# Kernel optimization log

Hardware: AMD Instinct MI355X
Metric: run time of the kernel (lower is better)

## Reference

```python
import jax, jax.numpy as jnp
import numpy as np

B, W = 256, 512
FEAT, TIME, OV_IN, OV = 128, 32, 32, 32
IN = FEAT + TIME + OV  # 192
HG, HL = 256, 128
OG, OL = 128, 64


def _p(key, shape, scale):
    return (jax.random.normal(key, shape, dtype=jnp.float32) * scale)


def setup_inputs() -> dict:
    key = jax.random.key(0)
    ks = jax.random.split(key, 24)
    d = {
        'f_seq': jax.random.normal(ks[0], (B, W, FEAT), dtype=jnp.float32),
        'delta_seq': jax.random.normal(ks[1], (B, W, TIME), dtype=jnp.float32),
        'overlap_seq': jax.random.normal(ks[2], (B, W, OV_IN), dtype=jnp.float32),
        # overlap encoder: Linear(32,64) -> SiLU -> Linear(64,32)
        'W1': _p(ks[3], (64, OV_IN), 1.0 / np.sqrt(OV_IN)),
        'b1': _p(ks[4], (64,), 0.02),
        'W2': _p(ks[5], (OV, 64), 1.0 / np.sqrt(64)),
        'b2': _p(ks[6], (OV,), 0.02),
        # global GRUCell (PyTorch layout: [r; z; n] stacked)
        'Wih_g': _p(ks[7], (3 * HG, IN), 1.0 / np.sqrt(HG)),
        'Whh_g': _p(ks[8], (3 * HG, HG), 1.0 / np.sqrt(HG)),
        'bih_g': _p(ks[9], (3 * HG,), 0.02),
        'bhh_g': _p(ks[10], (3 * HG,), 0.02),
        # local GRUCell
        'Wih_l': _p(ks[11], (3 * HL, IN), 1.0 / np.sqrt(HL)),
        'Whh_l': _p(ks[12], (3 * HL, HL), 1.0 / np.sqrt(HL)),
        'bih_l': _p(ks[13], (3 * HL,), 0.02),
        'bhh_l': _p(ks[14], (3 * HL,), 0.02),
        # output projections
        'Wg': _p(ks[15], (OG, HG), 1.0 / np.sqrt(HG)),
        'bg': _p(ks[16], (OG,), 0.02),
        'Wl': _p(ks[17], (OL, HL), 1.0 / np.sqrt(HL)),
        'bl': _p(ks[18], (OL,), 0.02),
    }
    return d


def _gru_scan(x_ih_seq, h0, Whh, bhh):
    # x_ih_seq: (W, B, 3H) precomputed input gates; returns hidden states (W, B, H)
    def step(h, xih):
        gh = h @ Whh.T + bhh
        xr, xz, xn = jnp.split(xih, 3, axis=-1)
        hr, hz, hn = jnp.split(gh, 3, axis=-1)
        r = jax.nn.sigmoid(xr + hr)
        z = jax.nn.sigmoid(xz + hz)
        n = jnp.tanh(xn + r * hn)
        h_new = (1.0 - z) * n + z * h
        return h_new, h_new
    _, hs = jax.lax.scan(step, h0, x_ih_seq)
    return hs


def _forward(f_seq, delta_seq, overlap_seq, W1, b1, W2, b2,
             Wih_g, Whh_g, bih_g, bhh_g, Wih_l, Whh_l, bih_l, bhh_l,
             Wg, bg, Wl, bl):
    # overlap encoder applied to whole sequence (time-independent)
    ov = jax.nn.silu(overlap_seq @ W1.T + b1) @ W2.T + b2  # (B, W, OV)
    inp = jnp.concatenate([f_seq, delta_seq, ov], axis=-1)  # (B, W, IN)
    # precompute input-to-hidden gates for all timesteps (batched GEMM)
    xih_g = (inp @ Wih_g.T + bih_g).transpose(1, 0, 2)  # (W, B, 3HG)
    xih_l = (inp @ Wih_l.T + bih_l).transpose(1, 0, 2)  # (W, B, 3HL)
    h_g0 = jnp.zeros((inp.shape[0], Whh_g.shape[1]), dtype=inp.dtype)
    h_l0 = jnp.zeros((inp.shape[0], Whh_l.shape[1]), dtype=inp.dtype)
    hg_seq = _gru_scan(xih_g, h_g0, Whh_g, bhh_g)  # (W, B, HG)
    hl_seq = _gru_scan(xih_l, h_l0, Whh_l, bhh_l)  # (W, B, HL)
    g_seq = (hg_seq @ Wg.T + bg).transpose(1, 0, 2)  # (B, W, OG)
    m_seq = (hl_seq @ Wl.T + bl).transpose(1, 0, 2)  # (B, W, OL)
    return g_seq, m_seq


def reference(f_seq, delta_seq, overlap_seq, W1, b1, W2, b2,
              Wih_g, Whh_g, bih_g, bhh_g, Wih_l, Whh_l, bih_l, bhh_l,
              Wg, bg, Wl, bl):
    return _forward(f_seq, delta_seq, overlap_seq, W1, b1, W2, b2,
                    Wih_g, Whh_g, bih_g, bhh_g, Wih_l, Whh_l, bih_l, bhh_l,
                    Wg, bg, Wl, bl)
```

## Files before the change

### kernel.cpp

```cpp
#include <hip/hip_runtime.h>

typedef _Float16 f16;
typedef _Float16 f16x2 __attribute__((ext_vector_type(2)));
typedef _Float16 f16x8 __attribute__((ext_vector_type(8)));
typedef float f32x4 __attribute__((ext_vector_type(4)));
typedef unsigned int u32;

static constexpr size_t NROWS = 131072;
static constexpr int TC = 64;
static constexpr int NCHUNK = 8;
static constexpr size_t CROWS = 256 * TC;

static constexpr size_t O_INP = 0;
static constexpr size_t SZ_INP = NROWS * 192 * 2;
static constexpr size_t O_XB  = O_INP + SZ_INP;
static constexpr size_t SZ_XB = CROWS * 1152 * 2;
static constexpr size_t O_HG  = O_XB + SZ_XB;
static constexpr size_t SZ_HG = NROWS * 256 * 2;
static constexpr size_t O_HL  = O_HG + SZ_HG;
static constexpr size_t SZ_HL = NROWS * 128 * 2;
static constexpr size_t O_WF  = O_HL + SZ_HL;
static constexpr size_t SZ_WF = 1152 * 192 * 2;
static constexpr size_t O_BF  = O_WF + SZ_WF;
static constexpr size_t SZ_BF = 1152 * 4;
static constexpr size_t O_WHG = O_BF + SZ_BF;
static constexpr size_t SZ_WHG = 128 * 768 * 4;
static constexpr size_t O_WHL = O_WHG + SZ_WHG;
static constexpr size_t SZ_WHL = 64 * 384 * 4;
static constexpr size_t O_WG  = O_WHL + SZ_WHL;
static constexpr size_t SZ_WG = 128 * 256 * 2;
static constexpr size_t O_WL  = O_WG + SZ_WG;
static constexpr size_t SZ_WL = 64 * 128 * 2;
static constexpr size_t O_HGF = O_WL + SZ_WL;
static constexpr size_t SZ_HGF = 256 * 256 * 4;
static constexpr size_t O_HGP = O_HGF + SZ_HGF;
static constexpr size_t SZ_HGP = 256 * 128 * 4;
static constexpr size_t O_HLF = O_HGP + SZ_HGP;
static constexpr size_t SZ_HLF = 256 * 128 * 4;
static constexpr size_t O_HLP = O_HLF + SZ_HLF;
static constexpr size_t SZ_HLP = 256 * 64 * 4;
static constexpr size_t WS_NEED = O_HLP + SZ_HLP;

__device__ inline u32 pk2f(float lo, float hi) {
  f16x2 t; t.x = (f16)lo; t.y = (f16)hi;
  return __builtin_bit_cast(u32, t);
}

#if defined(__has_builtin)
#if __has_builtin(__builtin_amdgcn_fdot2)
#define HAVE_FDOT2 1
#endif
#endif

__device__ inline float dot2f(u32 w, u32 h, float c) {
#ifdef HAVE_FDOT2
  return __builtin_amdgcn_fdot2(__builtin_bit_cast(f16x2, w),
                                __builtin_bit_cast(f16x2, h), c, false);
#else
  f16x2 a = __builtin_bit_cast(f16x2, w);
  f16x2 b = __builtin_bit_cast(f16x2, h);
  return c + (float)a.x * (float)b.x + (float)a.y * (float)b.y;
#endif
}

__device__ inline float sigf(float x) { return 1.f / (1.f + __expf(-x)); }
__device__ inline float tanhf_fast(float x) { return 1.f - 2.f / (1.f + __expf(2.f * x)); }

__global__ void prep_k(const float* __restrict__ Wih_g, const float* __restrict__ Wih_l,
                       const float* __restrict__ bih_g, const float* __restrict__ bih_l,
                       const float* __restrict__ Whh_g, const float* __restrict__ Whh_l,
                       const float* __restrict__ Wg, const float* __restrict__ Wl,
                       f16* __restrict__ wfused, float* __restrict__ biasf,
                       u32* __restrict__ whhg, u32* __restrict__ whhl,
                       f16* __restrict__ wg16, f16* __restrict__ wl16) {
  const int tid = blockIdx.x * blockDim.x + threadIdx.x;
  const int stride = gridDim.x * blockDim.x;
  for (int i = tid; i < 1152 * 192; i += stride) {
    int r = i / 192;
    wfused[i] = (f16)(r < 768 ? Wih_g[i] : Wih_l[i - 768 * 192]);
  }
  for (int i = tid; i < 1152; i += stride)
    biasf[i] = (i < 768) ? bih_g[i] : bih_l[i - 768];
  for (int i = tid; i < 128 * 768; i += stride) {
    int k2 = i / 768, r = i % 768;
    whhg[i] = pk2f(Whh_g[r * 256 + 2 * k2], Whh_g[r * 256 + 2 * k2 + 1]);
  }
  for (int i = tid; i < 64 * 384; i += stride) {
    int k2 = i / 384, r = i % 384;
    whhl[i] = pk2f(Whh_l[r * 128 + 2 * k2], Whh_l[r * 128 + 2 * k2 + 1]);
  }
  for (int i = tid; i < 128 * 256; i += stride) wg16[i] = (f16)Wg[i];
  for (int i = tid; i < 64 * 128; i += stride) wl16[i] = (f16)Wl[i];
}

__global__ __launch_bounds__(256) void copy_f_k(const float* __restrict__ f_seq,
                                                f16* __restrict__ inp) {
  const size_t idx = (size_t)blockIdx.x * 256 + threadIdx.x;
  const float4 v = reinterpret_cast<const float4*>(f_seq)[idx];
  const size_t row = idx >> 5, c4 = idx & 31;
  uint2 pr; pr.x = pk2f(v.x, v.y); pr.y = pk2f(v.z, v.w);
  *reinterpret_cast<uint2*>(reinterpret_cast<u32*>(inp) + row * 96 + 2 * c4) = pr;
}

__global__ __launch_bounds__(256) void copy_d_k(const float* __restrict__ delta,
                                                f16* __restrict__ inp) {
  const size_t idx = (size_t)blockIdx.x * 256 + threadIdx.x;
  const float4 v = reinterpret_cast<const float4*>(delta)[idx];
  const size_t row = idx >> 3, c4 = idx & 7;
  uint2 pr; pr.x = pk2f(v.x, v.y); pr.y = pk2f(v.z, v.w);
  *reinterpret_cast<uint2*>(reinterpret_cast<u32*>(inp) + row * 96 + 64 + 2 * c4) = pr;
}

__global__ __launch_bounds__(256) void ovenc_k(
    const float* __restrict__ ovin, const float* __restrict__ W1,
    const float* __restrict__ b1, const float* __restrict__ W2,
    const float* __restrict__ b2, f16* __restrict__ inp) {
  __shared__ float sW1[2048], sW2[2048], sb1[64], sb2[32];
  for (int i = threadIdx.x; i < 2048; i += 256) { sW1[i] = W1[i]; sW2[i] = W2[i]; }
  if (threadIdx.x < 64) sb1[threadIdx.x] = b1[threadIdx.x];
  if (threadIdx.x < 32) sb2[threadIdx.x] = b2[threadIdx.x];
  __syncthreads();
  const size_t row = (size_t)blockIdx.x * 256 + threadIdx.x;

  float ov[32];
  const float4* ovp = reinterpret_cast<const float4*>(ovin + row * 32);
#pragma unroll
  for (int i = 0; i < 8; ++i) {
    float4 v = ovp[i];
    ov[4 * i] = v.x; ov[4 * i + 1] = v.y; ov[4 * i + 2] = v.z; ov[4 * i + 3] = v.w;
  }
  float hb[64];
#pragma unroll
  for (int j = 0; j < 64; ++j) {
    float s = sb1[j];
#pragma unroll
    for (int k = 0; k < 32; ++k) s += sW1[j * 32 + k] * ov[k];
    hb[j] = s * sigf(s);
  }
  u32* orow = reinterpret_cast<u32*>(inp) + row * 96 + 80;
#pragma unroll
  for (int p = 0; p < 16; ++p) {
    float s0 = sb2[2 * p], s1 = sb2[2 * p + 1];
#pragma unroll
    for (int j = 0; j < 64; ++j) {
      s0 += sW2[(2 * p) * 64 + j] * hb[j];
      s1 += sW2[(2 * p + 1) * 64 + j] * hb[j];
    }
    orow[p] = pk2f(s0, s1);
  }
}

template <int K, int NROWSB, int NVALID, bool OUTF16, int LDC, bool REMAP>
__global__ __launch_bounds__(256, 2) void gemm_f16k(
    const f16* __restrict__ A, const f16* __restrict__ Bw,
    const float* __restrict__ bias, void* __restrict__ Cout, int t_base) {
  __shared__ alignas(16) f16 At[128 * 40];
  __shared__ alignas(16) f16 Bt[128 * 40];
  const int n0 = blockIdx.x * 128;
  const int m0 = blockIdx.y * 128;
  const int tid = threadIdx.x;
  const int l = tid & 63;
  const int w = tid >> 6;
  const int wm = w >> 1, wn = w & 1;
  const int srow = tid >> 2, schunk = tid & 3;

  f32x4 acc[4][4] = {};

  for (int k0 = 0; k0 < K; k0 += 32) {
#pragma unroll
    for (int hh = 0; hh < 2; ++hh) {
      int row = srow + hh * 64;
      int m = m0 + row;
      size_t g = REMAP ? ((size_t)(m & 255) * 512 + (size_t)t_base + (size_t)(m >> 8))
                       : (size_t)m;
      uint4 av = *reinterpret_cast<const uint4*>(A + g * K + k0 + schunk * 8);
      *reinterpret_cast<uint4*>(&At[row * 40 + schunk * 8]) = av;
      int nr = n0 + row;
      uint4 bv = make_uint4(0u, 0u, 0u, 0u);
      if (nr < NROWSB)
        bv = *reinterpret_cast<const uint4*>(Bw + (size_t)nr * K + k0 + schunk * 8);
      *reinterpret_cast<uint4*>(&Bt[row * 40 + schunk * 8]) = bv;
    }
    __syncthreads();
    f16x8 af[4], bf[4];
#pragma unroll
    for (int i = 0; i < 4; ++i) {
      af[i] = *reinterpret_cast<const f16x8*>(&At[(wm * 64 + i * 16 + (l & 15)) * 40 + (l >> 4) * 8]);
      bf[i] = *reinterpret_cast<const f16x8*>(&Bt[(wn * 64 + i * 16 + (l & 15)) * 40 + (l >> 4) * 8]);
    }
#pragma unroll
    for (int mi = 0; mi < 4; ++mi)
#pragma unroll
      for (int ni = 0; ni < 4; ++ni)
        acc[mi][ni] = __builtin_amdgcn_mfma_f32_16x16x32_f16(af[mi], bf[ni], acc[mi][ni], 0, 0, 0);
    __syncthreads();
  }

  const int mbase = m0 + wm * 64 + ((l >> 4) << 2);
  const int nbase = n0 + wn * 64 + (l & 15);
#pragma unroll
  for (int mi = 0; mi < 4; ++mi) {
#pragma unroll
    for (int ni = 0; ni < 4; ++ni) {
      int n = nbase + ni * 16;
      if (n < NVALID) {
        float bsv = bias[n];
#pragma unroll
        for (int q = 0; q < 4; ++q) {
          int m = mbase + mi * 16 + q;
          float v = acc[mi][ni][q] + bsv;
          if constexpr (OUTF16)
            reinterpret_cast<f16*>(Cout)[(size_t)m * LDC + n] = (f16)v;
          else
            reinterpret_cast<float*>(Cout)[(size_t)m * LDC + n] = v;
        }
      }
    }
  }
}

__global__ __launch_bounds__(768, 3) void gru_global_k(
    const u32* __restrict__ whh, const float* __restrict__ bhh,
    const f16* __restrict__ xbuf, u32* __restrict__ hseq,
    float* __restrict__ hstf, u32* __restrict__ hstp, int t0) {
  __shared__ alignas(16) u32 hpk[128];
  __shared__ float hfs[256];
  __shared__ float rz[512];
  const int b = blockIdx.x;
  const int r = threadIdx.x;

  u32 wv[128];
#pragma unroll
  for (int i = 0; i < 128; ++i) wv[i] = whh[i * 768 + r];
  const float bh = bhh[r];

  if (t0 == 0) {
    if (r < 256) hfs[r] = 0.f;
    if (r < 128) hpk[r] = 0u;
  } else {
    if (r < 256) hfs[r] = hstf[b * 256 + r];
    if (r < 128) hpk[r] = hstp[b * 128 + r];
  }
  __syncthreads();

  const f16* xp = xbuf + (size_t)b * 1152 + r;
  u32* hout = hseq + (size_t)b * 512 * 128 + (size_t)t0 * 128;
  float xv = (float)xp[0];

  for (int t = 0; t < TC; ++t) {
    float xnext = 0.f;
    if (t < TC - 1) xnext = (float)xp[(size_t)(t + 1) * 256 * 1152];

    float a0 = 0.f, a1 = 0.f, a2 = 0.f, a3 = 0.f;
#pragma unroll
    for (int q = 0; q < 32; ++q) {
      uint4 hq = reinterpret_cast<const uint4*>(hpk)[q];
      a0 = dot2f(wv[4 * q + 0], hq.x, a0);
      a1 = dot2f(wv[4 * q + 1], hq.y, a1);
      a2 = dot2f(wv[4 * q + 2], hq.z, a2);
      a3 = dot2f(wv[4 * q + 3], hq.w, a3);
    }
    float gh = ((a0 + a1) + (a2 + a3)) + bh;

    if (r < 512) rz[r] = sigf(xv + gh);
    __syncthreads();
    if (r >= 512) {
      int j = r - 512;
      float rv = rz[j];
      float zv = rz[256 + j];
      float nv = tanhf_fast(xv + rv * gh);
      float hold = hfs[j];
      float hnew = (1.f - zv) * nv + zv * hold;
      hfs[j] = hnew;
      float hpart = __shfl_xor(hnew, 1, 64);
      if ((j & 1) == 0) {
        u32 packed = pk2f(hnew, hpart);
        hpk[j >> 1] = packed;
        hout[(size_t)t * 128 + (j >> 1)] = packed;
      }
    }
    __syncthreads();
    xv = xnext;
  }
  if (r < 256) hstf[b * 256 + r] = hfs[r];
  if (r < 128) hstp[b * 128 + r] = hpk[r];
}

__global__ __launch_bounds__(384, 2) void gru_local_k(
    const u32* __restrict__ whh, const float* __restrict__ bhh,
    const f16* __restrict__ xbuf, u32* __restrict__ hseq,
    float* __restrict__ hstf, u32* __restrict__ hstp, int t0) {
  __shared__ alignas(16) u32 hpk[64];
  __shared__ float hfs[128];
  __shared__ float rz[256];
  const int b = blockIdx.x;
  const int r = threadIdx.x;

  u32 wv[64];
#pragma unroll
  for (int i = 0; i < 64; ++i) wv[i] = whh[i * 384 + r];
  const float bh = bhh[r];

  if (t0 == 0) {
    if (r < 128) hfs[r] = 0.f;
    if (r < 64) hpk[r] = 0u;
  } else {
    if (r < 128) hfs[r] = hstf[b * 128 + r];
    if (r < 64) hpk[r] = hstp[b * 64 + r];
  }
  __syncthreads();

  const f16* xp = xbuf + (size_t)b * 1152 + 768 + r;
  u32* hout = hseq + (size_t)b * 512 * 64 + (size_t)t0 * 64;
  float xv = (float)xp[0];

  for (int t = 0; t < TC; ++t) {
    float xnext = 0.f;
    if (t < TC - 1) xnext = (float)xp[(size_t)(t + 1) * 256 * 1152];

    float a0 = 0.f, a1 = 0.f, a2 = 0.f, a3 = 0.f;
#pragma unroll
    for (int q = 0; q < 16; ++q) {
      uint4 hq = reinterpret_cast<const uint4*>(hpk)[q];
      a0 = dot2f(wv[4 * q + 0], hq.x, a0);
      a1 = dot2f(wv[4 * q + 1], hq.y, a1);
      a2 = dot2f(wv[4 * q + 2], hq.z, a2);
      a3 = dot2f(wv[4 * q + 3], hq.w, a3);
    }
    float gh = ((a0 + a1) + (a2 + a3)) + bh;

    if (r < 256) rz[r] = sigf(xv + gh);
    __syncthreads();
    if (r >= 256) {
      int j = r - 256;
      float rv = rz[j];
      float zv = rz[128 + j];
      float nv = tanhf_fast(xv + rv * gh);
      float hold = hfs[j];
      float hnew = (1.f - zv) * nv + zv * hold;
      hfs[j] = hnew;
      float hpart = __shfl_xor(hnew, 1, 64);
      if ((j & 1) == 0) {
        u32 packed = pk2f(hnew, hpart);
        hpk[j >> 1] = packed;
        hout[(size_t)t * 64 + (j >> 1)] = packed;
      }
    }
    __syncthreads();
    xv = xnext;
  }
  if (r < 128) hstf[b * 128 + r] = hfs[r];
  if (r < 64) hstp[b * 64 + r] = hpk[r];
}

extern "C" void kernel_launch(void* const* d_in, const int* in_sizes, int n_in,
                              void* d_out, int out_size, void* d_ws, size_t ws_size,
                              hipStream_t stream) {
  (void)in_sizes; (void)n_in; (void)out_size;
  if (ws_size < WS_NEED) return;
  const float* f_seq = (const float*)d_in[0];
  const float* delta = (const float*)d_in[1];
  const float* ovseq = (const float*)d_in[2];
  const float* W1 = (const float*)d_in[3];
  const float* b1 = (const float*)d_in[4];
  const float* W2 = (const float*)d_in[5];
  const float* b2 = (const float*)d_in[6];
  const float* Wih_g = (const float*)d_in[7];
  const float* Whh_g = (const float*)d_in[8];
  const float* bih_g = (const float*)d_in[9];
  const float* bhh_g = (const float*)d_in[10];
  const float* Wih_l = (const float*)d_in[11];
  const float* Whh_l = (const float*)d_in[12];
  const float* bih_l = (const float*)d_in[13];
  const float* bhh_l = (const float*)d_in[14];
  const float* Wg = (const float*)d_in[15];
  const float* bg = (const float*)d_in[16];
  const float* Wl = (const float*)d_in[17];
  const float* bl = (const float*)d_in[18];

  char* ws = (char*)d_ws;
  f16* inp = (f16*)(ws + O_INP);
  f16* xbuf = (f16*)(ws + O_XB);
  f16* hg16 = (f16*)(ws + O_HG);
  f16* hl16 = (f16*)(ws + O_HL);
  f16* wfused = (f16*)(ws + O_WF);
  float* biasf = (float*)(ws + O_BF);
  u32* whhg = (u32*)(ws + O_WHG);
  u32* whhl = (u32*)(ws + O_WHL);
  f16* wg16 = (f16*)(ws + O_WG);
  f16* wl16 = (f16*)(ws + O_WL);
  float* hgf = (float*)(ws + O_HGF);
  u32* hgp = (u32*)(ws + O_HGP);
  float* hlf = (float*)(ws + O_HLF);
  u32* hlp = (u32*)(ws + O_HLP);

  float* outg = (float*)d_out;
  float* outm = outg + NROWS * 128;

  prep_k<<<dim3(256), dim3(256), 0, stream>>>(Wih_g, Wih_l, bih_g, bih_l, Whh_g, Whh_l,
                                              Wg, Wl, wfused, biasf, whhg, whhl, wg16, wl16);
  copy_f_k<<<dim3(NROWS * 32 / 256), dim3(256), 0, stream>>>(f_seq, inp);
  copy_d_k<<<dim3(NROWS * 8 / 256), dim3(256), 0, stream>>>(delta, inp);
  ovenc_k<<<dim3(512), dim3(256), 0, stream>>>(ovseq, W1, b1, W2, b2, inp);

  for (int c = 0; c < NCHUNK; ++c) {
    gemm_f16k<192, 1152, 1152, true, 1152, true><<<dim3(9, CROWS / 128), dim3(256), 0, stream>>>(
        inp, wfused, biasf, xbuf, c * TC);
    gru_global_k<<<dim3(256), dim3(768), 0, stream>>>(whhg, bhh_g, xbuf, (u32*)hg16, hgf, hgp, c * TC);
    gru_local_k<<<dim3(256), dim3(384), 0, stream>>>(whhl, bhh_l, xbuf, (u32*)hl16, hlf, hlp, c * TC);
  }

  gemm_f16k<256, 128, 128, false, 128, false><<<dim3(1, 1024), dim3(256), 0, stream>>>(hg16, wg16, bg, outg, 0);
  gemm_f16k<128, 64, 64, false, 64, false><<<dim3(1, 1024), dim3(256), 0, stream>>>(hl16, wl16, bl, outm, 0);
}
```

Measured before the change: 1.612 ms.

## Split GRU recurrent dot products across 4 lanes with shuffle reduction

Repacks the recurrent weight matrices so each group of 4 lanes jointly computes 4 gate rows, each lane reading a distinct quarter of the hidden state from LDS. Partial sums are combined with xor shuffles. This replaces broadcast LDS reads of the whole hidden vector with fewer, spread-out reads per lane. An empty asm pins the weights in VGPRs, and the local GRU occupancy hint goes from 2 to 3 blocks per CU. The cost is extra shuffle instructions and a select on the recurrent critical path.

```diff
diff --git a/kernel.cpp b/kernel.cpp
--- a/kernel.cpp
+++ b/kernel.cpp
@@ -81,13 +81,17 @@
   }
   for (int i = tid; i < 1152; i += stride)
     biasf[i] = (i < 768) ? bih_g[i] : bih_l[i - 768];
-  for (int i = tid; i < 128 * 768; i += stride) {
-    int k2 = i / 768, r = i % 768;
-    whhg[i] = pk2f(Whh_g[r * 256 + 2 * k2], Whh_g[r * 256 + 2 * k2 + 1]);
-  }
-  for (int i = tid; i < 64 * 384; i += stride) {
-    int k2 = i / 384, r = i % 384;
-    whhl[i] = pk2f(Whh_l[r * 128 + 2 * k2], Whh_l[r * 128 + 2 * k2 + 1]);
+  for (int idx = tid; idx < 128 * 768; idx += stride) {
+    int i = idx / 768, j = idx % 768;
+    int g = j >> 2, s = j & 3, m = i >> 5, q = i & 31;
+    int row = 4 * g + m, u = s * 32 + q;
+    whhg[idx] = pk2f(Whh_g[row * 256 + 2 * u], Whh_g[row * 256 + 2 * u + 1]);
+  }
+  for (int idx = tid; idx < 64 * 384; idx += stride) {
+    int i = idx / 384, j = idx % 384;
+    int g = j >> 2, s = j & 3, m = i >> 4, q = i & 15;
+    int row = 4 * g + m, u = s * 16 + q;
+    whhl[idx] = pk2f(Whh_l[row * 128 + 2 * u], Whh_l[row * 128 + 2 * u + 1]);
   }
   for (int i = tid; i < 128 * 256; i += stride) wg16[i] = (f16)Wg[i];
   for (int i = tid; i < 64 * 128; i += stride) wl16[i] = (f16)Wl[i];
@@ -228,10 +232,13 @@
   __shared__ float rz[512];
   const int b = blockIdx.x;
   const int r = threadIdx.x;
+  const int s = r & 3;
 
   u32 wv[128];
 #pragma unroll
   for (int i = 0; i < 128; ++i) wv[i] = whh[i * 768 + r];
+#pragma unroll
+  for (int i = 0; i < 128; ++i) asm volatile("" : "+v"(wv[i]));
   const float bh = bhh[r];
 
   if (t0 == 0) {
@@ -245,6 +252,7 @@
 
   const f16* xp = xbuf + (size_t)b * 1152 + r;
   u32* hout = hseq + (size_t)b * 512 * 128 + (size_t)t0 * 128;
+  const uint4* hpk4 = reinterpret_cast<const uint4*>(hpk);
   float xv = (float)xp[0];
 
   for (int t = 0; t < TC; ++t) {
@@ -253,14 +261,30 @@
 
     float a0 = 0.f, a1 = 0.f, a2 = 0.f, a3 = 0.f;
 #pragma unroll
-    for (int q = 0; q < 32; ++q) {
-      uint4 hq = reinterpret_cast<const uint4*>(hpk)[q];
-      a0 = dot2f(wv[4 * q + 0], hq.x, a0);
-      a1 = dot2f(wv[4 * q + 1], hq.y, a1);
-      a2 = dot2f(wv[4 * q + 2], hq.z, a2);
-      a3 = dot2f(wv[4 * q + 3], hq.w, a3);
-    }
-    float gh = ((a0 + a1) + (a2 + a3)) + bh;
+    for (int cc = 0; cc < 8; ++cc) {
+      uint4 hq = hpk4[s * 8 + cc];
+      a0 = dot2f(wv[0 * 32 + cc * 4 + 0], hq.x, a0);
+      a1 = dot2f(wv[1 * 32 + cc * 4 + 0], hq.x, a1);
+      a2 = dot2f(wv[2 * 32 + cc * 4 + 0], hq.x, a2);
+      a3 = dot2f(wv[3 * 32 + cc * 4 + 0], hq.x, a3);
+      a0 = dot2f(wv[0 * 32 + cc * 4 + 1], hq.y, a0);
+      a1 = dot2f(wv[1 * 32 + cc * 4 + 1], hq.y, a1);
+      a2 = dot2f(wv[2 * 32 + cc * 4 + 1], hq.y, a2);
+      a3 = dot2f(wv[3 * 32 + cc * 4 + 1], hq.y, a3);
+      a0 = dot2f(wv[0 * 32 + cc * 4 + 2], hq.z, a0);
+      a1 = dot2f(wv[1 * 32 + cc * 4 + 2], hq.z, a1);
+      a2 = dot2f(wv[2 * 32 + cc * 4 + 2], hq.z, a2);
+      a3 = dot2f(wv[3 * 32 + cc * 4 + 2], hq.z, a3);
+      a0 = dot2f(wv[0 * 32 + cc * 4 + 3], hq.w, a0);
+      a1 = dot2f(wv[1 * 32 + cc * 4 + 3], hq.w, a1);
+      a2 = dot2f(wv[2 * 32 + cc * 4 + 3], hq.w, a2);
+      a3 = dot2f(wv[3 * 32 + cc * 4 + 3], hq.w, a3);
+    }
+    a0 += __shfl_xor(a0, 1, 64); a1 += __shfl_xor(a1, 1, 64);
+    a2 += __shfl_xor(a2, 1, 64); a3 += __shfl_xor(a3, 1, 64);
+    a0 += __shfl_xor(a0, 2, 64); a1 += __shfl_xor(a1, 2, 64);
+    a2 += __shfl_xor(a2, 2, 64); a3 += __shfl_xor(a3, 2, 64);
+    float gh = (s == 0 ? a0 : s == 1 ? a1 : s == 2 ? a2 : a3) + bh;
 
     if (r < 512) rz[r] = sigf(xv + gh);
     __syncthreads();
@@ -286,7 +310,7 @@
   if (r < 128) hstp[b * 128 + r] = hpk[r];
 }
 
-__global__ __launch_bounds__(384, 2) void gru_local_k(
+__global__ __launch_bounds__(384, 3) void gru_local_k(
     const u32* __restrict__ whh, const float* __restrict__ bhh,
     const f16* __restrict__ xbuf, u32* __restrict__ hseq,
     float* __restrict__ hstf, u32* __restrict__ hstp, int t0) {
@@ -295,10 +319,13 @@
   __shared__ float rz[256];
   const int b = blockIdx.x;
   const int r = threadIdx.x;
+  const int s = r & 3;
 
   u32 wv[64];
 #pragma unroll
   for (int i = 0; i < 64; ++i) wv[i] = whh[i * 384 + r];
+#pragma unroll
+  for (int i = 0; i < 64; ++i) asm volatile("" : "+v"(wv[i]));
   const float bh = bhh[r];
 
   if (t0 == 0) {
@@ -312,6 +339,7 @@
 
   const f16* xp = xbuf + (size_t)b * 1152 + 768 + r;
   u32* hout = hseq + (size_t)b * 512 * 64 + (size_t)t0 * 64;
+  const uint4* hpk4 = reinterpret_cast<const uint4*>(hpk);
   float xv = (float)xp[0];
 
   for (int t = 0; t < TC; ++t) {
@@ -320,14 +348,30 @@
 
     float a0 = 0.f, a1 = 0.f, a2 = 0.f, a3 = 0.f;
 #pragma unroll
-    for (int q = 0; q < 16; ++q) {
-      uint4 hq = reinterpret_cast<const uint4*>(hpk)[q];
-      a0 = dot2f(wv[4 * q + 0], hq.x, a0);
-      a1 = dot2f(wv[4 * q + 1], hq.y, a1);
-      a2 = dot2f(wv[4 * q + 2], hq.z, a2);
-      a3 = dot2f(wv[4 * q + 3], hq.w, a3);
-    }
-    float gh = ((a0 + a1) + (a2 + a3)) + bh;
+    for (int cc = 0; cc < 4; ++cc) {
+      uint4 hq = hpk4[s * 4 + cc];
+      a0 = dot2f(wv[0 * 16 + cc * 4 + 0], hq.x, a0);
+      a1 = dot2f(wv[1 * 16 + cc * 4 + 0], hq.x, a1);
+      a2 = dot2f(wv[2 * 16 + cc * 4 + 0], hq.x, a2);
+      a3 = dot2f(wv[3 * 16 + cc * 4 + 0], hq.x, a3);
+      a0 = dot2f(wv[0 * 16 + cc * 4 + 1], hq.y, a0);
+      a1 = dot2f(wv[1 * 16 + cc * 4 + 1], hq.y, a1);
+      a2 = dot2f(wv[2 * 16 + cc * 4 + 1], hq.y, a2);
+      a3 = dot2f(wv[3 * 16 + cc * 4 + 1], hq.y, a3);
+      a0 = dot2f(wv[0 * 16 + cc * 4 + 2], hq.z, a0);
+      a1 = dot2f(wv[1 * 16 + cc * 4 + 2], hq.z, a1);
+      a2 = dot2f(wv[2 * 16 + cc * 4 + 2], hq.z, a2);
+      a3 = dot2f(wv[3 * 16 + cc * 4 + 2], hq.z, a3);
+      a0 = dot2f(wv[0 * 16 + cc * 4 + 3], hq.w, a0);
+      a1 = dot2f(wv[1 * 16 + cc * 4 + 3], hq.w, a1);
+      a2 = dot2f(wv[2 * 16 + cc * 4 + 3], hq.w, a2);
+      a3 = dot2f(wv[3 * 16 + cc * 4 + 3], hq.w, a3);
+    }
+    a0 += __shfl_xor(a0, 1, 64); a1 += __shfl_xor(a1, 1, 64);
+    a2 += __shfl_xor(a2, 1, 64); a3 += __shfl_xor(a3, 1, 64);
+    a0 += __shfl_xor(a0, 2, 64); a1 += __shfl_xor(a1, 2, 64);
+    a2 += __shfl_xor(a2, 2, 64); a3 += __shfl_xor(a3, 2, 64);
+    float gh = (s == 0 ? a0 : s == 1 ? a1 : s == 2 ? a2 : a3) + bh;
 
     if (r < 256) rz[r] = sigf(xv + gh);
     __syncthreads();
```

New measurement: 1.786 ms. 1.11x slower.
